# Kernel optimization log

Measured on AMD Instinct MI355X. Metric: run time of the kernel, lower is better.

Reference implementation:

```python
import jax, jax.numpy as jnp
import numpy as np

TEMPERATURE = 0.2
NUMBER_CLASSES = 1000
LOSS_SCALE = 0.001

N, F = 8192, 256
M = 20000
DEPTH = 4


def setup_inputs() -> dict:
    key = jax.random.key(0)
    k1, k2, k3, k4 = jax.random.split(key, 4)
    gt_labels = jax.random.randint(k1, (N,), 0, NUMBER_CLASSES, dtype=jnp.int32)
    box_features = jax.random.normal(k2, (N, F), dtype=jnp.float32)
    memory = jax.random.normal(k3, (M, F), dtype=jnp.float32)
    trace_idx = jax.random.randint(k4, (NUMBER_CLASSES, DEPTH), 0, M, dtype=jnp.int32)
    return {"gt_labels": gt_labels, "box_features": box_features,
            "memory": memory, "trace_idx": trace_idx}


def reference(gt_labels, box_features, memory, trace_idx):
    # logits[i, j] = dot(f_i, m_j) / T  (the nested python loops fused into one GEMM)
    logits = jnp.einsum('nf,mf->nm', box_features, memory) / TEMPERATURE  # [N, M]
    # fenmu = sum_j exp(logits)  ->  log(fenmu) = logsumexp
    lse = jax.nn.logsumexp(logits, axis=-1)  # [N]
    # gather the trace entries for each item's label: [N, DEPTH]
    traces = trace_idx[gt_labels]  # [N, DEPTH]
    sel = jnp.take_along_axis(logits, traces, axis=1)  # [N, DEPTH]
    depth_w = jnp.arange(DEPTH, dtype=logits.dtype)  # gj = depth
    sum_gj = depth_w.sum()  # sum of layer weights (0+1+2+3)
    # per item: -sum_d gj * log(sim_d / fenmu) / sum_gj
    per_item = -jnp.sum((sel - lse[:, None]) * depth_w, axis=-1) / sum_gj  # [N]
    # background filter: items with label == number_classes contribute nothing
    fg = (gt_labels != NUMBER_CLASSES)
    loss = jnp.sum(jnp.where(fg, per_item, 0.0)) * LOSS_SCALE
    return loss
```

## Files before the change

kernel.cpp:

```cpp
#include <hip/hip_runtime.h>
#include <hip/hip_bf16.h>
#include <stdint.h>

#define NROWS 8192
#define FDIM 256
#define MCOLS 20000
#define NT32 625
#define MSPLIT 8
#define NCLS 1000
#define LOG2E 1.44269504088896f
#define LN2   0.69314718055994f


typedef short short8 __attribute__((ext_vector_type(8)));
typedef float f32x16 __attribute__((ext_vector_type(16)));

typedef __attribute__((address_space(3))) unsigned int lds_u32;
typedef const __attribute__((address_space(1))) unsigned int glb_u32;

__device__ __forceinline__ float ex2(float x) {
    float r;
    asm("v_exp_f32 %0, %1" : "=v"(r) : "v"(x));
    return r;
}

__device__ __forceinline__ unsigned short f2bf(float x) {
    unsigned u = __float_as_uint(x);
    unsigned r = (u + 0x7FFFu + ((u >> 16) & 1u)) >> 16;
    return (unsigned short)r;
}

__device__ __forceinline__ float vmax16(f32x16 v) {
    float x0 = fmaxf(fmaxf(v[0],  v[1]),  v[2]);
    float x1 = fmaxf(fmaxf(v[3],  v[4]),  v[5]);
    float x2 = fmaxf(fmaxf(v[6],  v[7]),  v[8]);
    float x3 = fmaxf(fmaxf(v[9],  v[10]), v[11]);
    float x4 = fmaxf(fmaxf(v[12], v[13]), v[14]);
    float x5 = fmaxf(fmaxf(x0, x1), x2);
    float x6 = fmaxf(fmaxf(x3, x4), v[15]);
    return fmaxf(x5, x6);
}

__global__ void prep_kernel(const float* __restrict__ Mem, unsigned short* __restrict__ Mb2,
                            const float* __restrict__ F, unsigned short* __restrict__ Fb,
                            const int* __restrict__ gt, const int* __restrict__ trace,
                            float* __restrict__ wsel) {
    int b = blockIdx.x;
    if (b < 2500) {
        int g = b * 256 + threadIdx.x;
        int s = g & 63, kk = (g >> 6) & 15, t = g >> 10;
        const float* src = Mem + (size_t)(t * 32 + (s & 31)) * FDIM + kk * 16 + (s >> 5) * 8;
        float4 v0 = ((const float4*)src)[0];
        float4 v1 = ((const float4*)src)[1];
        short8 w;
        w[0] = (short)f2bf(v0.x); w[1] = (short)f2bf(v0.y);
        w[2] = (short)f2bf(v0.z); w[3] = (short)f2bf(v0.w);
        w[4] = (short)f2bf(v1.x); w[5] = (short)f2bf(v1.y);
        w[6] = (short)f2bf(v1.z); w[7] = (short)f2bf(v1.w);
        *(short8*)(Mb2 + (size_t)g * 8) = w;
    } else if (b < 4548) {
        int idx = (b - 2500) * 256 + threadIdx.x;
        float4 v = ((const float4*)F)[idx];
        const float sc = 5.0f * LOG2E;
        ushort4 o;
        o.x = f2bf(v.x * sc); o.y = f2bf(v.y * sc);
        o.z = f2bf(v.z * sc); o.w = f2bf(v.w * sc);
        ((ushort4*)Fb)[idx] = o;
    } else {
        int lane = threadIdx.x & 63, wid = threadIdx.x >> 6;
        int i = (b - 4548) * 4 + wid;
        int label = gt[i];
        float w = 0.0f;
        if (label >= 0 && label < NCLS) {
            float4 fv = ((const float4*)(F + (size_t)i * FDIM))[lane];
            #pragma unroll
            for (int d = 1; d <= 3; ++d) {
                int tr = trace[label * 4 + d];
                float4 mv = ((const float4*)(Mem + (size_t)tr * FDIM))[lane];
                float dot = fv.x*mv.x + fv.y*mv.y + fv.z*mv.z + fv.w*mv.w;
                #pragma unroll
                for (int off = 32; off >= 1; off >>= 1) dot += __shfl_xor(dot, off, 64);
                w += (float)d * dot;
            }
        }
        if (lane == 0) wsel[i] = w * 5.0f;
    }
}

__global__ __attribute__((amdgpu_flat_work_group_size(256, 256), amdgpu_waves_per_eu(1, 1)))
void lse_gemm(
        const unsigned short* __restrict__ Fb, const unsigned short* __restrict__ Mb2,
        float* __restrict__ pm, float* __restrict__ ps) {
    __shared__ __align__(16) char smem[2 * 16384];

    const int split  = blockIdx.x;
    const int rowblk = blockIdx.y;
    const int tid  = threadIdx.x;
    const int lane = tid & 63, wid = tid >> 6;
    const int r0 = lane & 31;
    const int hi = lane >> 5;
    const int rowbase = rowblk * 256 + wid * 64;
    const int l16 = lane << 4;

    short8 al[16], ah[16];
    #pragma unroll
    for (int kk = 0; kk < 16; ++kk) {
        al[kk] = *(const short8*)(Fb + (size_t)(rowbase + r0)      * FDIM + kk * 16 + hi * 8);
        ah[kk] = *(const short8*)(Fb + (size_t)(rowbase + 32 + r0) * FDIM + kk * 16 + hi * 8);
    }

    float m0 = -3.0e38f, s0 = 0.0f, m1 = -3.0e38f, s1 = 0.0f;
    float nmL, nmH, q0, q1, q2, q3, r0x, r1x, r2x, r3x;
    f32x16 accLA, accHA, accLB, accHB;

    const int t0 = (split * NT32) / MSPLIT;
    const int t1 = ((split + 1) * NT32) / MSPLIT;

#define STAGE(BUF, t)                                                              \
    do {                                                                           \
        const char* srcT = (const char*)Mb2 + (size_t)(t) * 16384 + l16;           \
        _Pragma("unroll")                                                          \
        for (int c = 0; c < 4; ++c) {                                              \
            __builtin_amdgcn_global_load_lds(                                      \
                (glb_u32*)(srcT + (wid * 4 + c) * 1024),                           \
                (lds_u32*)(smem + (BUF) * 16384 + (wid * 4 + c) * 1024),           \
                16, 0, 0);                                                         \
        }                                                                          \
    } while (0)

#define MFMA_K(BP, CUR, KK)                                                        \
    {                                                                              \
        short8 b_ = *(const short8*)((BP) + (KK) * 1024);                          \
        accL##CUR = __builtin_amdgcn_mfma_f32_32x32x16_bf16(b_, al[KK], accL##CUR, 0, 0, 0); \
        accH##CUR = __builtin_amdgcn_mfma_f32_32x32x16_bf16(b_, ah[KK], accH##CUR, 0, 0, 0); \
    }

#define SM_P0(P)                                                                   \
    nmL = fmaxf(vmax16(accL##P), m0); nmH = fmaxf(vmax16(accH##P), m1);            \
    q0 = q1 = q2 = q3 = 0.f; r0x = r1x = r2x = r3x = 0.f;

#define SM_P1(P)                                                                   \
    q0 += ex2(accL##P[0] - nmL); q1 += ex2(accL##P[1] - nmL);                      \
    q2 += ex2(accL##P[2] - nmL); q3 += ex2(accL##P[3] - nmL);                      \
    q0 += ex2(accL##P[4] - nmL); q1 += ex2(accL##P[5] - nmL);                      \
    q2 += ex2(accL##P[6] - nmL); q3 += ex2(accL##P[7] - nmL);

#define SM_P2(P)                                                                   \
    q0 += ex2(accL##P[8]  - nmL); q1 += ex2(accL##P[9]  - nmL);                    \
    q2 += ex2(accL##P[10] - nmL); q3 += ex2(accL##P[11] - nmL);                    \
    q0 += ex2(accL##P[12] - nmL); q1 += ex2(accL##P[13] - nmL);                    \
    q2 += ex2(accL##P[14] - nmL); q3 += ex2(accL##P[15] - nmL);                    \
    s0 = fmaf(s0, ex2(m0 - nmL), (q0 + q1) + (q2 + q3)); m0 = nmL;

#define SM_P3(P)                                                                   \
    r0x += ex2(accH##P[0]  - nmH); r1x += ex2(accH##P[1]  - nmH);                  \
    r2x += ex2(accH##P[2]  - nmH); r3x += ex2(accH##P[3]  - nmH);                  \
    r0x += ex2(accH##P[4]  - nmH); r1x += ex2(accH##P[5]  - nmH);                  \
    r2x += ex2(accH##P[6]  - nmH); r3x += ex2(accH##P[7]  - nmH);                  \
    r0x += ex2(accH##P[8]  - nmH); r1x += ex2(accH##P[9]  - nmH);                  \
    r2x += ex2(accH##P[10] - nmH); r3x += ex2(accH##P[11] - nmH);                  \
    r0x += ex2(accH##P[12] - nmH); r1x += ex2(accH##P[13] - nmH);                  \
    r2x += ex2(accH##P[14] - nmH); r3x += ex2(accH##P[15] - nmH);                  \
    s1 = fmaf(s1, ex2(m1 - nmH), (r0x + r1x) + (r2x + r3x)); m1 = nmH;

#define PIPE(BUF, CUR, PRV)                                                        \
    do {                                                                           \
        const char* bp_ = smem + (BUF) * 16384 + l16;                              \
        f32x16 z_ = {0,0,0,0,0,0,0,0,0,0,0,0,0,0,0,0};                             \
        accL##CUR = z_; accH##CUR = z_;                                            \
        _Pragma("unroll") for (int kk = 0;  kk < 4;  ++kk) MFMA_K(bp_, CUR, kk)    \
        SM_P0(PRV)                                                                 \
        _Pragma("unroll") for (int kk = 4;  kk < 8;  ++kk) MFMA_K(bp_, CUR, kk)    \
        SM_P1(PRV)                                                                 \
        _Pragma("unroll") for (int kk = 8;  kk < 12; ++kk) MFMA_K(bp_, CUR, kk)    \
        SM_P2(PRV)                                                                 \
        _Pragma("unroll") for (int kk = 12; kk < 16; ++kk) MFMA_K(bp_, CUR, kk)    \
        SM_P3(PRV)                                                                 \
    } while (0)

#define MFMA_ONLY(BUF, CUR)                                                        \
    do {                                                                           \
        const char* bp_ = smem + (BUF) * 16384 + l16;                              \
        f32x16 z_ = {0,0,0,0,0,0,0,0,0,0,0,0,0,0,0,0};                             \
        accL##CUR = z_; accH##CUR = z_;                                            \
        _Pragma("unroll") for (int kk = 0; kk < 16; ++kk) MFMA_K(bp_, CUR, kk)     \
    } while (0)

#define SM_FULL(P) do { SM_P0(P) SM_P1(P) SM_P2(P) SM_P3(P) } while (0)

    STAGE(0, t0);
    __syncthreads();
    STAGE(1, t0 + 1);
    MFMA_ONLY(0, A);
    __syncthreads();

    int t = t0 + 1;
    while (t + 2 <= t1) {
        STAGE(0, t + 1);
        PIPE(1, B, A);
        __syncthreads();
        if (t + 2 < t1) STAGE(1, t + 2);
        PIPE(0, A, B);
        __syncthreads();
        t += 2;
    }
    if (t < t1) {
        PIPE(1, B, A);
        SM_FULL(B);
    } else {
        SM_FULL(A);
    }

#undef SM_FULL
#undef MFMA_ONLY
#undef PIPE
#undef SM_P3
#undef SM_P2
#undef SM_P1
#undef SM_P0
#undef MFMA_K
#undef STAGE

    {
        float om = __shfl_xor(m0, 32, 64);
        float os = __shfl_xor(s0, 32, 64);
        float nm = fmaxf(m0, om);
        float sf = fmaf(s0, ex2(m0 - nm), os * ex2(om - nm));
        if (lane < 32) {
            pm[split * NROWS + rowbase + lane] = nm;
            ps[split * NROWS + rowbase + lane] = sf;
        }
    }
    {
        float om = __shfl_xor(m1, 32, 64);
        float os = __shfl_xor(s1, 32, 64);
        float nm = fmaxf(m1, om);
        float sf = fmaf(s1, ex2(m1 - nm), os * ex2(om - nm));
        if (lane < 32) {
            pm[split * NROWS + rowbase + 32 + lane] = nm;
            ps[split * NROWS + rowbase + 32 + lane] = sf;
        }
    }
}

__global__ void finalize_kernel(const int* __restrict__ gt, const float* __restrict__ wsel,
                                const float* __restrict__ pm, const float* __restrict__ ps,
                                float* __restrict__ bpart) {
    int tid = threadIdx.x;
    int i = blockIdx.x * 256 + tid;
    float mv[MSPLIT];
    float M = -3.0e38f;
    #pragma unroll
    for (int k = 0; k < MSPLIT; ++k) { mv[k] = pm[k * NROWS + i]; M = fmaxf(M, mv[k]); }
    float S = 0.0f;
    #pragma unroll
    for (int k = 0; k < MSPLIT; ++k) S += ps[k * NROWS + i] * ex2(mv[k] - M);
    float lse = (M + __log2f(S)) * LN2;
    int label = gt[i];
    float per = (label >= 0 && label < NCLS) ? (lse - wsel[i] * (1.0f / 6.0f)) : 0.0f;
    #pragma unroll
    for (int off = 32; off >= 1; off >>= 1) per += __shfl_xor(per, off, 64);
    __shared__ float red[4];
    int lane = tid & 63, wid = tid >> 6;
    if (lane == 0) red[wid] = per;
    __syncthreads();
    if (tid == 0) bpart[blockIdx.x] = red[0] + red[1] + red[2] + red[3];
}

__global__ void sum_kernel(const float* __restrict__ bpart, float* __restrict__ out) {
    int tid = threadIdx.x;
    float v = (tid < 32) ? bpart[tid] : 0.0f;
    #pragma unroll
    for (int off = 32; off >= 1; off >>= 1) v += __shfl_xor(v, off, 64);
    if (tid == 0) out[0] = 0.001f * v;
}

extern "C" void kernel_launch(void* const* d_in, const int* in_sizes, int n_in,
                              void* d_out, int out_size, void* d_ws, size_t ws_size,
                              hipStream_t stream) {
    const int*   gt    = (const int*)d_in[0];
    const float* F     = (const float*)d_in[1];
    const float* Mem   = (const float*)d_in[2];
    const int*   trace = (const int*)d_in[3];
    float* out = (float*)d_out;

    char* w = (char*)d_ws;
    unsigned short* Mb2 = (unsigned short*)w;
    unsigned short* Fb  = (unsigned short*)(w + 10240000);
    float* wsel  = (float*)(w + 14434304);
    float* pm    = (float*)(w + 14467072);
    float* ps    = (float*)(w + 14991360);
    float* bpart = (float*)(w + 15515648);

    prep_kernel<<<dim3(6596), dim3(256), 0, stream>>>(Mem, Mb2, F, Fb, gt, trace, wsel);
    lse_gemm<<<dim3(MSPLIT, NROWS / 256), dim3(256), 0, stream>>>(Fb, Mb2, pm, ps);
    finalize_kernel<<<dim3(NROWS / 256), dim3(256), 0, stream>>>(gt, wsel, pm, ps, bpart);
    sum_kernel<<<dim3(1), dim3(64), 0, stream>>>(bpart, out);
}
```

Baseline: 98.68 us.

## Load memory tiles directly into registers instead of staging through LDS

The B operand tiles, which are shared by the four waves in a block, are no longer staged into LDS with global_load_lds and synchronized with barriers. Each wave now loads the full 16 KB tile into two register double-buffers (b0/b1) straight from global memory. This removes the LDS round trip and the __syncthreads calls, but every wave now fetches the same tile, so global/L2 traffic rises about fourfold and register pressure grows by 128 VGPRs.

```diff
diff --git a/kernel.cpp b/kernel.cpp
--- a/kernel.cpp
+++ b/kernel.cpp
@@ -14,9 +14,6 @@
 
 typedef short short8 __attribute__((ext_vector_type(8)));
 typedef float f32x16 __attribute__((ext_vector_type(16)));
-
-typedef __attribute__((address_space(3))) unsigned int lds_u32;
-typedef const __attribute__((address_space(1))) unsigned int glb_u32;
 
 __device__ __forceinline__ float ex2(float x) {
     float r;
@@ -91,8 +88,6 @@
 void lse_gemm(
         const unsigned short* __restrict__ Fb, const unsigned short* __restrict__ Mb2,
         float* __restrict__ pm, float* __restrict__ ps) {
-    __shared__ __align__(16) char smem[2 * 16384];
-
     const int split  = blockIdx.x;
     const int rowblk = blockIdx.y;
     const int tid  = threadIdx.x;
@@ -112,27 +107,23 @@
     float m0 = -3.0e38f, s0 = 0.0f, m1 = -3.0e38f, s1 = 0.0f;
     float nmL, nmH, q0, q1, q2, q3, r0x, r1x, r2x, r3x;
     f32x16 accLA, accHA, accLB, accHB;
+    short8 b0[16], b1[16];
 
     const int t0 = (split * NT32) / MSPLIT;
     const int t1 = ((split + 1) * NT32) / MSPLIT;
 
-#define STAGE(BUF, t)                                                              \
+#define LOADB(BB, t)                                                               \
     do {                                                                           \
-        const char* srcT = (const char*)Mb2 + (size_t)(t) * 16384 + l16;           \
+        const char* srcT_ = (const char*)Mb2 + (size_t)(t) * 16384 + l16;          \
         _Pragma("unroll")                                                          \
-        for (int c = 0; c < 4; ++c) {                                              \
-            __builtin_amdgcn_global_load_lds(                                      \
-                (glb_u32*)(srcT + (wid * 4 + c) * 1024),                           \
-                (lds_u32*)(smem + (BUF) * 16384 + (wid * 4 + c) * 1024),           \
-                16, 0, 0);                                                         \
-        }                                                                          \
+        for (int kk = 0; kk < 16; ++kk)                                            \
+            BB[kk] = *(const short8*)(srcT_ + kk * 1024);                          \
     } while (0)
 
-#define MFMA_K(BP, CUR, KK)                                                        \
+#define MFMA_K(BB, CUR, KK)                                                        \
     {                                                                              \
-        short8 b_ = *(const short8*)((BP) + (KK) * 1024);                          \
-        accL##CUR = __builtin_amdgcn_mfma_f32_32x32x16_bf16(b_, al[KK], accL##CUR, 0, 0, 0); \
-        accH##CUR = __builtin_amdgcn_mfma_f32_32x32x16_bf16(b_, ah[KK], accH##CUR, 0, 0, 0); \
+        accL##CUR = __builtin_amdgcn_mfma_f32_32x32x16_bf16(BB[KK], al[KK], accL##CUR, 0, 0, 0); \
+        accH##CUR = __builtin_amdgcn_mfma_f32_32x32x16_bf16(BB[KK], ah[KK], accH##CUR, 0, 0, 0); \
     }
 
 #define SM_P0(P)                                                                   \
@@ -163,49 +154,43 @@
     r2x += ex2(accH##P[14] - nmH); r3x += ex2(accH##P[15] - nmH);                  \
     s1 = fmaf(s1, ex2(m1 - nmH), (r0x + r1x) + (r2x + r3x)); m1 = nmH;
 
-#define PIPE(BUF, CUR, PRV)                                                        \
+#define PIPE(BB, CUR, PRV)                                                         \
     do {                                                                           \
-        const char* bp_ = smem + (BUF) * 16384 + l16;                              \
         f32x16 z_ = {0,0,0,0,0,0,0,0,0,0,0,0,0,0,0,0};                             \
         accL##CUR = z_; accH##CUR = z_;                                            \
-        _Pragma("unroll") for (int kk = 0;  kk < 4;  ++kk) MFMA_K(bp_, CUR, kk)    \
+        _Pragma("unroll") for (int kk = 0;  kk < 4;  ++kk) MFMA_K(BB, CUR, kk)     \
         SM_P0(PRV)                                                                 \
-        _Pragma("unroll") for (int kk = 4;  kk < 8;  ++kk) MFMA_K(bp_, CUR, kk)    \
+        _Pragma("unroll") for (int kk = 4;  kk < 8;  ++kk) MFMA_K(BB, CUR, kk)     \
         SM_P1(PRV)                                                                 \
-        _Pragma("unroll") for (int kk = 8;  kk < 12; ++kk) MFMA_K(bp_, CUR, kk)    \
+        _Pragma("unroll") for (int kk = 8;  kk < 12; ++kk) MFMA_K(BB, CUR, kk)     \
         SM_P2(PRV)                                                                 \
-        _Pragma("unroll") for (int kk = 12; kk < 16; ++kk) MFMA_K(bp_, CUR, kk)    \
+        _Pragma("unroll") for (int kk = 12; kk < 16; ++kk) MFMA_K(BB, CUR, kk)     \
         SM_P3(PRV)                                                                 \
     } while (0)
 
-#define MFMA_ONLY(BUF, CUR)                                                        \
+#define MFMA_ONLY(BB, CUR)                                                         \
     do {                                                                           \
-        const char* bp_ = smem + (BUF) * 16384 + l16;                              \
         f32x16 z_ = {0,0,0,0,0,0,0,0,0,0,0,0,0,0,0,0};                             \
         accL##CUR = z_; accH##CUR = z_;                                            \
-        _Pragma("unroll") for (int kk = 0; kk < 16; ++kk) MFMA_K(bp_, CUR, kk)     \
+        _Pragma("unroll") for (int kk = 0; kk < 16; ++kk) MFMA_K(BB, CUR, kk)      \
     } while (0)
 
 #define SM_FULL(P) do { SM_P0(P) SM_P1(P) SM_P2(P) SM_P3(P) } while (0)
 
-    STAGE(0, t0);
-    __syncthreads();
-    STAGE(1, t0 + 1);
-    MFMA_ONLY(0, A);
-    __syncthreads();
+    LOADB(b0, t0);
+    LOADB(b1, t0 + 1);
+    MFMA_ONLY(b0, A);
 
     int t = t0 + 1;
-    while (t + 2 <= t1) {
-        STAGE(0, t + 1);
-        PIPE(1, B, A);
-        __syncthreads();
-        if (t + 2 < t1) STAGE(1, t + 2);
-        PIPE(0, A, B);
-        __syncthreads();
+    while (t + 1 < t1) {
+        LOADB(b0, t + 1);
+        PIPE(b1, B, A);
+        if (t + 2 < t1) LOADB(b1, t + 2);
+        PIPE(b0, A, B);
         t += 2;
     }
     if (t < t1) {
-        PIPE(1, B, A);
+        PIPE(b1, B, A);
         SM_FULL(B);
     } else {
         SM_FULL(A);
@@ -219,7 +204,7 @@
 #undef SM_P1
 #undef SM_P0
 #undef MFMA_K
-#undef STAGE
+#undef LOADB
 
     {
         float om = __shfl_xor(m0, 32, 64);
```

Measured after the change: 96.95 us, median of 2. About the same (-1.7%).
